# Performance work log

Measured on AMD Instinct MI355X. Metric: run time of the kernel, lower is better.

The kernel has to match this reference:

```python
import jax, jax.numpy as jnp
import numpy as np

B, T, D = 8, 1024, 512
H = 8
F_OUT = D // H          # 64 per head
ALPHA = 0.2             # LeakyReLU slope in GAT
MASK_RATE = 0.3
GAMMA = 0.0625          # DistanceAdj gamma
BIAS = 0.2              # DistanceAdj bias
LN_EPS = 1e-5
NEG_INF = -9e15
L2_EPS = 1e-12          # F.normalize eps


def setup_inputs() -> dict:
    key = jax.random.key(0)
    ks = jax.random.split(key, 8)
    return {
        "x": jax.random.normal(ks[0], (B, T, D), jnp.float32),
        "W": jax.random.normal(ks[1], (H, D, F_OUT), jnp.float32) * 0.05,
        "a_src": jax.random.normal(ks[2], (H, F_OUT), jnp.float32) * 0.05,
        "a_dst": jax.random.normal(ks[3], (H, F_OUT), jnp.float32) * 0.05,
        "W2": jax.random.normal(ks[4], (D, D), jnp.float32) * 0.02,
        "b2": jnp.zeros((D,), jnp.float32),
        "ln_g": jnp.ones((D,), jnp.float32),
        "ln_b": jnp.zeros((D,), jnp.float32),
    }


def _distance_adj(batch, t):
    # DistanceAdj: Gaussian kernel over temporal index distance, shared across batch
    idx = jnp.arange(t, dtype=jnp.float32)
    d2 = (idx[:, None] - idx[None, :]) ** 2
    adj = jnp.exp(-GAMMA * d2 - BIAS)                      # [T, T]
    return jnp.broadcast_to(adj[None], (batch, t, t))      # [B, T, T]


def reference(x, W, a_src, a_dst, W2, b2, ln_g, ln_b):
    b, t, d = x.shape
    adj = _distance_adj(b, t)

    # top-k magnitude node selection -> row/col union mask (index_fill loop)
    k = int(MASK_RATE * t)
    mags = jnp.linalg.norm(x, axis=2)                      # [B, T]
    _, topk = jax.lax.top_k(mags, k)                       # [B, k]
    sel = jnp.zeros((b, t), bool).at[jnp.arange(b)[:, None], topk].set(True)
    mask = sel[:, :, None] | sel[:, None, :]               # rows OR cols filled
    adj = jnp.where(mask, adj, 0.0)

    # GAT multi-head attention (dense masked form, dropout=0 at eval)
    Wh = jnp.einsum("btd,hdf->bhtf", x, W)                 # [B,H,T,F']
    e_src = jnp.einsum("bhtf,hf->bht", Wh, a_src)
    e_dst = jnp.einsum("bhtf,hf->bht", Wh, a_dst)
    e = jax.nn.leaky_relu(e_src[..., :, None] + e_dst[..., None, :], ALPHA)
    e = jnp.where(adj[:, None] > 0, e, NEG_INF)            # masked logits
    attn = jax.nn.softmax(e, axis=-1)                      # [B,H,T,T]
    hp = jnp.einsum("bhts,bhsf->bhtf", attn, Wh)
    hp = jax.nn.elu(hp)                                    # concat=True -> elu per head
    tmp = hp.transpose(0, 2, 1, 3).reshape(b, t, d)        # concat heads -> [B,T,512]

    # signed-sqrt + F.normalize (default dim=1 -> over T axis)
    tmp = jnp.sqrt(jax.nn.relu(tmp)) - jnp.sqrt(jax.nn.relu(-tmp))
    nrm = jnp.linalg.norm(tmp, axis=1, keepdims=True)      # [B,1,D]
    tmp = tmp / jnp.maximum(nrm, L2_EPS)

    # residual linear + LayerNorm + permute
    y = x + tmp @ W2 + b2
    mu = jnp.mean(y, axis=-1, keepdims=True)
    var = jnp.mean((y - mu) ** 2, axis=-1, keepdims=True)
    y = (y - mu) / jnp.sqrt(var + LN_EPS) * ln_g + ln_b
    return y.transpose(0, 2, 1)                            # [B, D, T]
```

## Files before the change

### kernel.cpp

```cpp
#include <hip/hip_runtime.h>
#include <hip/hip_bf16.h>

typedef unsigned short u16;
typedef short bf16x8 __attribute__((ext_vector_type(8)));
typedef float f32x4 __attribute__((ext_vector_type(4)));
typedef int   i32x4 __attribute__((ext_vector_type(4)));

#define NB 8
#define NT 1024
#define ND 512
#define KSEL 307
#define PSTR 152
#define TSTR 136

__device__ __forceinline__ float bf2f(u16 u){
  union { unsigned int i; float f; } c; c.i = ((unsigned int)u) << 16; return c.f;
}
__device__ __forceinline__ u16 f2bf(float f){
  __hip_bfloat16 h = __float2bfloat16(f);
  u16 u; __builtin_memcpy(&u, &h, 2); return u;
}

__global__ void k_convert_w(const float* __restrict__ W, const float* __restrict__ W2,
                            u16* __restrict__ WcatT, u16* __restrict__ W2T){
  int idx = blockIdx.x * 256 + threadIdx.x;
  if (idx < 262144){
    int c = idx >> 9, d = idx & 511;
    int src = ((c >> 6) << 15) | (d << 6) | (c & 63);
    WcatT[idx] = f2bf(W[src]);
  } else {
    int i = idx - 262144;
    int n = i >> 9, k = i & 511;
    W2T[i] = f2bf(W2[(k << 9) | n]);
  }
}

__global__ void k_select(const float* __restrict__ mags, int* __restrict__ sel){
  __shared__ float sm[NT];
  int b = blockIdx.x;
  int tid = threadIdx.x;
  for (int i = tid; i < NT; i += 256) sm[i] = mags[b * NT + i];
  __syncthreads();
  int tl = tid >> 2, tq = tid & 3;
  int t = blockIdx.y * 64 + tl;
  float m = sm[t];
  int cnt = 0;
  int s0 = tq * 256;
  for (int s = s0; s < s0 + 256; s++){
    float v = sm[s];
    cnt += (v > m) || (v == m && s < t);
  }
  cnt += __shfl_xor(cnt, 1, 64);
  cnt += __shfl_xor(cnt, 2, 64);
  if (tq == 0) sel[b * NT + t] = (cnt < KSEL) ? 1 : 0;
}

__launch_bounds__(256, 3)
__global__ void k_gemm_wh(const float* __restrict__ x, const u16* __restrict__ Bt,
                          const float* __restrict__ a_src, const float* __restrict__ a_dst,
                          u16* __restrict__ WhT, float* __restrict__ es, float* __restrict__ ed,
                          float* __restrict__ mags){
  __shared__ u16 smem[8704];
  u16* As = smem;
  u16* Bs = smem + 5120;
  int m0 = blockIdx.x * 128;
  int h  = blockIdx.y;
  int tid = threadIdx.x;
  int wv = tid >> 6, lane = tid & 63;
  int quad = lane >> 4, lr = lane & 15;
  f32x4 acc[2][4] = {};
  float sq[2] = {0.f, 0.f};
  for (int kt = 0; kt < 512; kt += 32){
    __syncthreads();
#pragma unroll
    for (int i = 0; i < 2; i++){
      int e = tid * 8 + i * 2048;
      int r = e >> 5, c = e & 31;
      const float* xa = &x[(m0 + r) * 512 + kt + c];
      f32x4 u0 = *(const f32x4*)xa;
      f32x4 u1 = *(const f32x4*)(xa + 4);
      u16 pk[8];
#pragma unroll
      for (int q = 0; q < 4; q++){
        sq[i] += u0[q]*u0[q] + u1[q]*u1[q];
        pk[q] = f2bf(u0[q]); pk[4+q] = f2bf(u1[q]);
      }
      *(bf16x8*)&As[r*40 + c] = *(const bf16x8*)pk;
    }
    {
      int e = tid * 8;
      int r = e >> 5, c = e & 31;
      *(bf16x8*)&Bs[r*40 + c] = *(const bf16x8*)&Bt[(h * 64 + r) * 512 + kt + c];
    }
    __syncthreads();
    bf16x8 af[2], bfr[4];
#pragma unroll
    for (int i = 0; i < 2; i++) af[i] = *(const bf16x8*)&As[(wv*32 + i*16 + lr)*40 + quad*8];
#pragma unroll
    for (int i = 0; i < 4; i++) bfr[i] = *(const bf16x8*)&Bs[(i*16 + lr)*40 + quad*8];
#pragma unroll
    for (int mi = 0; mi < 2; mi++)
#pragma unroll
      for (int ni = 0; ni < 4; ni++)
        acc[mi][ni] = __builtin_amdgcn_mfma_f32_16x16x32_bf16(af[mi], bfr[ni], acc[mi][ni], 0, 0, 0);
  }
  if (blockIdx.y == 0){
#pragma unroll
    for (int i = 0; i < 2; i++){
      float s = sq[i];
      s += __shfl_xor(s, 1, 64);
      s += __shfl_xor(s, 2, 64);
      if ((tid & 3) == 0) mags[m0 + i*64 + (tid >> 2)] = sqrtf(s);
    }
  }
  float asv[4], adv[4];
#pragma unroll
  for (int ni = 0; ni < 4; ni++){
    asv[ni] = a_src[h*64 + ni*16 + lr];
    adv[ni] = a_dst[h*64 + ni*16 + lr];
  }
#pragma unroll
  for (int mi = 0; mi < 2; mi++)
#pragma unroll
    for (int r = 0; r < 4; r++){
      float pes = 0.f, ped = 0.f;
#pragma unroll
      for (int ni = 0; ni < 4; ni++){
        pes += acc[mi][ni][r] * asv[ni];
        ped += acc[mi][ni][r] * adv[ni];
      }
#pragma unroll
      for (int mofs = 1; mofs < 16; mofs <<= 1){
        pes += __shfl_xor(pes, mofs, 64);
        ped += __shfl_xor(ped, mofs, 64);
      }
      if (lr == 0){
        int rowg = m0 + wv*32 + mi*16 + quad*4 + r;
        int bb_ = rowg >> 10, tt = rowg & 1023;
        es[(bb_ * 8 + h) * NT + tt] = pes;
        ed[(bb_ * 8 + h) * NT + tt] = ped;
      }
    }
  __syncthreads();
  u16* Tr = smem;
#pragma unroll
  for (int mi = 0; mi < 2; mi++)
#pragma unroll
    for (int ni = 0; ni < 4; ni++){
      int fl = ni*16 + lr;
      int tl = wv*32 + mi*16 + quad*4;
#pragma unroll
      for (int r = 0; r < 4; r++) Tr[fl*TSTR + tl + r] = f2bf(acc[mi][ni][r]);
    }
  __syncthreads();
  int f = tid >> 2, seg = tid & 3;
  int b_ = m0 >> 10;
  u16* dst = &WhT[(b_ * 512 + h * 64 + f) * NT + (m0 & 1023) + seg*32];
  const u16* srcp = &Tr[f*TSTR + seg*32];
#pragma unroll
  for (int k8 = 0; k8 < 4; k8++)
    *(bf16x8*)(dst + k8*8) = *(const bf16x8*)(srcp + k8*8);
}

__launch_bounds__(256)
__global__ void k_attn(const u16* __restrict__ WhT, const float* __restrict__ es,
                       const float* __restrict__ ed, const int* __restrict__ sel,
                       u16* __restrict__ t2b, float* __restrict__ cn){
  __shared__ u16 P[64 * PSTR];
  __shared__ float edw[144];
  __shared__ int   selw[144];
  __shared__ float esw[64];
  __shared__ float swv[64];
  int bh = blockIdx.x;
  int b = bh >> 3;
  int t0 = blockIdx.y * 64;
  int tid = threadIdx.x;
  int wv = tid >> 6, lane = tid & 63;
  int quad = lane >> 4, lr = lane & 15;
  int s_base = t0 - 40;
  for (int i = tid; i < 144; i += 256){
    int s = s_base + i;
    bool ok = (s >= 0 && s < NT);
    edw[i]  = ok ? ed[bh * NT + s] : 0.f;
    selw[i] = ok ? sel[b * NT + s] : 0;
  }
  if (tid < 64) esw[tid] = es[bh * NT + t0 + tid];
  {
    i32x4 z = {};
    for (int i = lane; i < 304; i += 64){
      int r16 = i / 19, c16 = i - r16 * 19;
      *(i32x4*)&P[(16*wv + r16) * PSTR + c16 * 8] = z;
    }
  }
  __syncthreads();
  {
    int tl = 16*wv + (lane >> 2);
    int q = lane & 3;
    float e_t = esw[tl];
    int sel_t = selw[tl + 40];
    float part = 0.f;
    for (int j = q; j <= 80; j += 4){
      int sw = tl + j;
      int s = s_base + sw;
      float w = 0.f;
      if (s >= 0 && s < NT && (sel_t | selw[sw])){
        float v = e_t + edw[sw];
        v = v > 0.f ? v : 0.2f * v;
        v = fminf(v, 60.f);
        w = bf2f(f2bf(__expf(v)));
      }
      part += w;
      if (w != 0.f) P[tl * PSTR + sw] = f2bf(w);
    }
    part += __shfl_xor(part, 1, 64);
    part += __shfl_xor(part, 2, 64);
    if (q == 0) swv[tl] = part;
  }
  f32x4 acc[4] = {};
  const u16* vbase = WhT + (bh * 64) * NT;
#pragma unroll
  for (int ks = 0; ks < 96; ks += 32){
    bf16x8 afr = *(const bf16x8*)&P[(16*wv + lr) * PSTR + 16*wv + ks + quad*8];
    int tb = s_base + 16*wv + ks + quad*8;
    bool ok = (tb >= 0) && (tb < NT);
    bf16x8 zf = {};
#pragma unroll
    for (int jn = 0; jn < 4; jn++){
      bf16x8 bfr = ok ? *(const bf16x8*)&vbase[(16*jn + lr) * NT + tb] : zf;
      acc[jn] = __builtin_amdgcn_mfma_f32_16x16x32_bf16(afr, bfr, acc[jn], 0, 0, 0);
    }
  }
#pragma unroll
  for (int jn = 0; jn < 4; jn++){
    float ssum = 0.f;
#pragma unroll
    for (int r = 0; r < 4; r++){
      int t_loc = 16*wv + quad*4 + r;
      float sw_ = swv[t_loc];
      float hp = acc[jn][r] / (sw_ > 0.f ? sw_ : 1.f);
      hp = hp > 0.f ? hp : (__expf(hp) - 1.f);
      float o = hp >= 0.f ? sqrtf(hp) : -sqrtf(-hp);
      ssum += o * o;
      t2b[(b * NT + t0 + t_loc) * ND + (bh & 7) * 64 + 16*jn + lr] = f2bf(o);
    }
    ssum += __shfl_xor(ssum, 16, 64);
    ssum += __shfl_xor(ssum, 32, 64);
    if (quad == 0) atomicAdd(&cn[b * ND + (bh & 7) * 64 + 16*jn + lr], ssum);
  }
}

__launch_bounds__(256, 3)
__global__ void k_gemm2(const u16* __restrict__ A, const u16* __restrict__ Bt,
                        const float* __restrict__ xres, const float* __restrict__ b2,
                        const float* __restrict__ cn, float* __restrict__ Y,
                        float* __restrict__ rsum, float* __restrict__ rqsum){
  __shared__ u16 As[128 * 40];
  __shared__ u16 Bs[64 * 40];
  __shared__ float scl[512];
  int m0 = blockIdx.x * 128, n0 = blockIdx.y * 64;
  int tid = threadIdx.x;
  int wv = tid >> 6, lane = tid & 63;
  int quad = lane >> 4, lr = lane & 15;
  int bb0 = (m0 >> 10) << 9;
  for (int i = tid; i < 512; i += 256){
    float nv = sqrtf(cn[bb0 + i]);
    scl[i] = 1.f / fmaxf(nv, 1e-12f);
  }
  f32x4 acc[2][4] = {};
  for (int kt = 0; kt < 512; kt += 32){
    __syncthreads();
#pragma unroll
    for (int i = 0; i < 2; i++){
      int e = tid * 8 + i * 2048;
      int r = e >> 5, c = e & 31;
      bf16x8 raw = *(const bf16x8*)&A[(m0 + r) * 512 + kt + c];
      u16 pk[8];
#pragma unroll
      for (int q = 0; q < 8; q++)
        pk[q] = f2bf(bf2f((u16)raw[q]) * scl[kt + c + q]);
      *(bf16x8*)&As[r*40 + c] = *(const bf16x8*)pk;
    }
    {
      int e = tid * 8;
      int r = e >> 5, c = e & 31;
      *(bf16x8*)&Bs[r*40 + c] = *(const bf16x8*)&Bt[(n0 + r) * 512 + kt + c];
    }
    __syncthreads();
    bf16x8 af[2], bfr[4];
#pragma unroll
    for (int i = 0; i < 2; i++) af[i] = *(const bf16x8*)&As[(wv*32 + i*16 + lr)*40 + quad*8];
#pragma unroll
    for (int i = 0; i < 4; i++) bfr[i] = *(const bf16x8*)&Bs[(i*16 + lr)*40 + quad*8];
#pragma unroll
    for (int mi = 0; mi < 2; mi++)
#pragma unroll
      for (int ni = 0; ni < 4; ni++)
        acc[mi][ni] = __builtin_amdgcn_mfma_f32_16x16x32_bf16(af[mi], bfr[ni], acc[mi][ni], 0, 0, 0);
  }
  float b2v[4];
#pragma unroll
  for (int ni = 0; ni < 4; ni++) b2v[ni] = b2[n0 + ni*16 + lr];
#pragma unroll
  for (int mi = 0; mi < 2; mi++){
    int rgb = m0 + wv*32 + mi*16 + quad*4;
#pragma unroll
    for (int r = 0; r < 4; r++){
      int row = rgb + r;
      float rs = 0.f, rq = 0.f;
#pragma unroll
      for (int ni = 0; ni < 4; ni++){
        int cg = n0 + ni*16 + lr;
        int idx = row * 512 + cg;
        float yv = acc[mi][ni][r] + xres[idx] + b2v[ni];
        Y[idx] = yv;
        rs += yv; rq += yv * yv;
      }
#pragma unroll
      for (int m2 = 1; m2 < 16; m2 <<= 1){
        rs += __shfl_xor(rs, m2, 64);
        rq += __shfl_xor(rq, m2, 64);
      }
      if (lr == 0){
        atomicAdd(&rsum[row], rs);
        atomicAdd(&rqsum[row], rq);
      }
    }
  }
}

__global__ void k_outln(const float* __restrict__ Y, const float* __restrict__ rsum,
                        const float* __restrict__ rqsum, const float* __restrict__ g,
                        const float* __restrict__ bb, float* __restrict__ out){
  __shared__ float mus[64], rss[64];
  __shared__ float tile[64 * 65];
  int t0 = blockIdx.x * 64, b = blockIdx.y;
  int cbase = blockIdx.z * 128;
  int tid = threadIdx.x;
  if (tid < 64){
    int row = b * NT + t0 + tid;
    float m = rsum[row] * (1.f/512.f);
    float var = rqsum[row] * (1.f/512.f) - m * m;
    mus[tid] = m;
    rss[tid] = 1.f / sqrtf(var + 1e-5f);
  }
  __syncthreads();
  int j = tid & 63, i0 = tid >> 6;
  for (int c0 = cbase; c0 < cbase + 128; c0 += 64){
#pragma unroll
    for (int k = 0; k < 16; k++){
      int i = i0 + k * 4;
      float v = (Y[(b * NT + t0 + i) * ND + c0 + j] - mus[i]) * rss[i] * g[c0 + j] + bb[c0 + j];
      tile[i * 65 + j] = v;
    }
    __syncthreads();
#pragma unroll
    for (int k = 0; k < 16; k++){
      int jj = i0 + k * 4;
      out[(b * ND + c0 + jj) * NT + t0 + j] = tile[j * 65 + jj];
    }
    __syncthreads();
  }
}

extern "C" void kernel_launch(void* const* d_in, const int* in_sizes, int n_in,
                              void* d_out, int out_size, void* d_ws, size_t ws_size,
                              hipStream_t stream) {
  (void)in_sizes; (void)n_in; (void)out_size; (void)ws_size;
  const float* x     = (const float*)d_in[0];
  const float* W     = (const float*)d_in[1];
  const float* a_src = (const float*)d_in[2];
  const float* a_dst = (const float*)d_in[3];
  const float* W2    = (const float*)d_in[4];
  const float* b2    = (const float*)d_in[5];
  const float* ln_g  = (const float*)d_in[6];
  const float* ln_b  = (const float*)d_in[7];
  char* ws = (char*)d_ws;
  int*   sel   = (int*)  (ws + 256);
  float* mags  = (float*)(ws + 33024);
  u16*   WcatT = (u16*)  (ws + 65792);
  u16*   W2T   = (u16*)  (ws + 590080);
  float* es    = (float*)(ws + 1124608);
  float* ed    = (float*)(ws + 1386752);
  float* cn    = (float*)(ws + 1648896);
  float* rsum  = (float*)(ws + 1665280);
  float* rqsum = (float*)(ws + 1698048);
  u16*   WhT   = (u16*)  (ws + 2097152);
  u16*   t2b   = (u16*)  (ws + 18874368);
  float* Y     = (float*)(ws + 2097152);
  float* out   = (float*)d_out;

  k_convert_w<<<2048, 256, 0, stream>>>(W, W2, WcatT, W2T);
  hipMemsetAsync(cn, 0, 81920, stream);
  k_gemm_wh  <<<dim3(64, 8), 256, 0, stream>>>(x, WcatT, a_src, a_dst, WhT, es, ed, mags);
  k_select   <<<dim3(NB, 16), 256, 0, stream>>>(mags, sel);
  k_attn     <<<dim3(64, 16), 256, 0, stream>>>(WhT, es, ed, sel, t2b, cn);
  k_gemm2    <<<dim3(64, 8), 256, 0, stream>>>(t2b, W2T, x, b2, cn, Y, rsum, rqsum);
  k_outln    <<<dim3(16, NB, 4), 256, 0, stream>>>(Y, rsum, rqsum, ln_g, ln_b, out);
}
```

Measured before the change: 161.1 us.

## Fuse second GEMM with LayerNorm and transposed output write

Replaces the tiled output-projection GEMM plus separate LayerNorm/transpose kernel with one kernel in which each block computes full 512-wide rows for 32 tokens. The row statistics are reduced in shared memory instead of with global atomics, and the normalized tile is transposed through LDS and written out directly. This removes the Y intermediate round trip, the atomics and one launch. In exchange the grid shrinks to 256 blocks, each block re-streams all of W2, and LDS usage rises, lowering occupancy.

```diff
diff --git a/kernel.cpp b/kernel.cpp
--- a/kernel.cpp
+++ b/kernel.cpp
@@ -12,6 +12,8 @@
 #define KSEL 307
 #define PSTR 152
 #define TSTR 136
+#define AS2 520
+#define BS2 36
 
 __device__ __forceinline__ float bf2f(u16 u){
   union { unsigned int i; float f; } c; c.i = ((unsigned int)u) << 16; return c.f;
@@ -249,116 +251,133 @@
   }
 }
 
-__launch_bounds__(256, 3)
-__global__ void k_gemm2(const u16* __restrict__ A, const u16* __restrict__ Bt,
-                        const float* __restrict__ xres, const float* __restrict__ b2,
-                        const float* __restrict__ cn, float* __restrict__ Y,
-                        float* __restrict__ rsum, float* __restrict__ rqsum){
-  __shared__ u16 As[128 * 40];
-  __shared__ u16 Bs[64 * 40];
+__launch_bounds__(256, 2)
+__global__ void k_gemm2out(const u16* __restrict__ A, const u16* __restrict__ Bt,
+                           const float* __restrict__ xres, const float* __restrict__ b2,
+                           const float* __restrict__ cn, const float* __restrict__ g,
+                           const float* __restrict__ bb, float* __restrict__ out){
+  __shared__ i32x4 smemQ[4384];
   __shared__ float scl[512];
-  int m0 = blockIdx.x * 128, n0 = blockIdx.y * 64;
+  __shared__ float sS[128], sQ[128];
+  __shared__ float mus[32], rss[32];
+  u16* As = (u16*)smemQ;
+  u16* Bs = (u16*)smemQ + 16640;
+  float* tile = (float*)smemQ;
+  int m0 = blockIdx.x * 32;
+  int b  = m0 >> 10;
+  int t0 = m0 & 1023;
   int tid = threadIdx.x;
-  int wv = tid >> 6, lane = tid & 63;
+  int w = tid >> 6, lane = tid & 63;
   int quad = lane >> 4, lr = lane & 15;
-  int bb0 = (m0 >> 10) << 9;
+  int bb0 = b << 9;
   for (int i = tid; i < 512; i += 256){
     float nv = sqrtf(cn[bb0 + i]);
     scl[i] = 1.f / fmaxf(nv, 1e-12f);
   }
-  f32x4 acc[2][4] = {};
+  __syncthreads();
+  {
+    int row = tid >> 3, seg = tid & 7;
+    const u16* src = &A[(size_t)(m0 + row) * 512 + seg * 64];
+    u16* dstl = &As[row * AS2 + seg * 64];
+#pragma unroll
+    for (int j = 0; j < 8; j++){
+      bf16x8 raw = *(const bf16x8*)(src + j*8);
+      u16 pk[8];
+#pragma unroll
+      for (int e = 0; e < 8; e++)
+        pk[e] = f2bf(bf2f((u16)raw[e]) * scl[seg*64 + j*8 + e]);
+      *(bf16x8*)(dstl + j*8) = *(const bf16x8*)pk;
+    }
+  }
+  f32x4 acc[2][8] = {};
   for (int kt = 0; kt < 512; kt += 32){
     __syncthreads();
 #pragma unroll
-    for (int i = 0; i < 2; i++){
-      int e = tid * 8 + i * 2048;
-      int r = e >> 5, c = e & 31;
-      bf16x8 raw = *(const bf16x8*)&A[(m0 + r) * 512 + kt + c];
-      u16 pk[8];
-#pragma unroll
-      for (int q = 0; q < 8; q++)
-        pk[q] = f2bf(bf2f((u16)raw[q]) * scl[kt + c + q]);
-      *(bf16x8*)&As[r*40 + c] = *(const bf16x8*)pk;
-    }
-    {
-      int e = tid * 8;
-      int r = e >> 5, c = e & 31;
-      *(bf16x8*)&Bs[r*40 + c] = *(const bf16x8*)&Bt[(n0 + r) * 512 + kt + c];
+    for (int half = 0; half < 2; half++){
+      int n = tid + half*256;
+      const u16* src = &Bt[(size_t)n * 512 + kt];
+      u16* dstl = &Bs[n * BS2];
+#pragma unroll
+      for (int j = 0; j < 4; j++)
+        *(bf16x8*)(dstl + j*8) = *(const bf16x8*)(src + j*8);
     }
     __syncthreads();
-    bf16x8 af[2], bfr[4];
-#pragma unroll
-    for (int i = 0; i < 2; i++) af[i] = *(const bf16x8*)&As[(wv*32 + i*16 + lr)*40 + quad*8];
-#pragma unroll
-    for (int i = 0; i < 4; i++) bfr[i] = *(const bf16x8*)&Bs[(i*16 + lr)*40 + quad*8];
-#pragma unroll
-    for (int mi = 0; mi < 2; mi++)
-#pragma unroll
-      for (int ni = 0; ni < 4; ni++)
-        acc[mi][ni] = __builtin_amdgcn_mfma_f32_16x16x32_bf16(af[mi], bfr[ni], acc[mi][ni], 0, 0, 0);
-  }
-  float b2v[4];
-#pragma unroll
-  for (int ni = 0; ni < 4; ni++) b2v[ni] = b2[n0 + ni*16 + lr];
-#pragma unroll
-  for (int mi = 0; mi < 2; mi++){
-    int rgb = m0 + wv*32 + mi*16 + quad*4;
+    bf16x8 af0 = *(const bf16x8*)&As[lr * AS2 + kt + quad*8];
+    bf16x8 af1 = *(const bf16x8*)&As[(16 + lr) * AS2 + kt + quad*8];
+#pragma unroll
+    for (int ni = 0; ni < 8; ni++){
+      bf16x8 bfr = *(const bf16x8*)&Bs[(w*128 + ni*16 + lr)*BS2 + quad*8];
+      acc[0][ni] = __builtin_amdgcn_mfma_f32_16x16x32_bf16(af0, bfr, acc[0][ni], 0, 0, 0);
+      acc[1][ni] = __builtin_amdgcn_mfma_f32_16x16x32_bf16(af1, bfr, acc[1][ni], 0, 0, 0);
+    }
+  }
+  float b2v[8];
+#pragma unroll
+  for (int ni = 0; ni < 8; ni++) b2v[ni] = b2[w*128 + ni*16 + lr];
+#pragma unroll
+  for (int mi = 0; mi < 2; mi++)
 #pragma unroll
     for (int r = 0; r < 4; r++){
-      int row = rgb + r;
+      int row = mi*16 + quad*4 + r;
       float rs = 0.f, rq = 0.f;
 #pragma unroll
-      for (int ni = 0; ni < 4; ni++){
-        int cg = n0 + ni*16 + lr;
-        int idx = row * 512 + cg;
-        float yv = acc[mi][ni][r] + xres[idx] + b2v[ni];
-        Y[idx] = yv;
+      for (int ni = 0; ni < 8; ni++){
+        int col = w*128 + ni*16 + lr;
+        float yv = acc[mi][ni][r] + xres[(size_t)(m0 + row) * 512 + col] + b2v[ni];
+        acc[mi][ni][r] = yv;
         rs += yv; rq += yv * yv;
       }
 #pragma unroll
-      for (int m2 = 1; m2 < 16; m2 <<= 1){
-        rs += __shfl_xor(rs, m2, 64);
-        rq += __shfl_xor(rq, m2, 64);
-      }
-      if (lr == 0){
-        atomicAdd(&rsum[row], rs);
-        atomicAdd(&rqsum[row], rq);
-      }
-    }
-  }
-}
-
-__global__ void k_outln(const float* __restrict__ Y, const float* __restrict__ rsum,
-                        const float* __restrict__ rqsum, const float* __restrict__ g,
-                        const float* __restrict__ bb, float* __restrict__ out){
-  __shared__ float mus[64], rss[64];
-  __shared__ float tile[64 * 65];
-  int t0 = blockIdx.x * 64, b = blockIdx.y;
-  int cbase = blockIdx.z * 128;
-  int tid = threadIdx.x;
-  if (tid < 64){
-    int row = b * NT + t0 + tid;
-    float m = rsum[row] * (1.f/512.f);
-    float var = rqsum[row] * (1.f/512.f) - m * m;
+      for (int mo = 1; mo < 16; mo <<= 1){
+        rs += __shfl_xor(rs, mo, 64);
+        rq += __shfl_xor(rq, mo, 64);
+      }
+      if (lr == 0){ sS[row*4 + w] = rs; sQ[row*4 + w] = rq; }
+    }
+  __syncthreads();
+  if (tid < 32){
+    float s = sS[tid*4] + sS[tid*4+1] + sS[tid*4+2] + sS[tid*4+3];
+    float q = sQ[tid*4] + sQ[tid*4+1] + sQ[tid*4+2] + sQ[tid*4+3];
+    float m = s * (1.f/512.f);
+    float var = q * (1.f/512.f) - m * m;
     mus[tid] = m;
     rss[tid] = 1.f / sqrtf(var + 1e-5f);
   }
   __syncthreads();
-  int j = tid & 63, i0 = tid >> 6;
-  for (int c0 = cbase; c0 < cbase + 128; c0 += 64){
-#pragma unroll
-    for (int k = 0; k < 16; k++){
-      int i = i0 + k * 4;
-      float v = (Y[(b * NT + t0 + i) * ND + c0 + j] - mus[i]) * rss[i] * g[c0 + j] + bb[c0 + j];
-      tile[i * 65 + j] = v;
-    }
-    __syncthreads();
-#pragma unroll
-    for (int k = 0; k < 16; k++){
-      int jj = i0 + k * 4;
-      out[(b * ND + c0 + jj) * NT + t0 + j] = tile[j * 65 + jj];
-    }
-    __syncthreads();
+  float gv[8], bv[8];
+#pragma unroll
+  for (int ni = 0; ni < 8; ni++){
+    gv[ni] = g[w*128 + ni*16 + lr];
+    bv[ni] = bb[w*128 + ni*16 + lr];
+  }
+#pragma unroll
+  for (int mi = 0; mi < 2; mi++)
+#pragma unroll
+    for (int r = 0; r < 4; r++){
+      int row = mi*16 + quad*4 + r;
+      float mu_ = mus[row], rs_ = rss[row];
+#pragma unroll
+      for (int ni = 0; ni < 8; ni++){
+        int col = w*128 + ni*16 + lr;
+        tile[col*33 + row] = (acc[mi][ni][r] - mu_) * rs_ * gv[ni] + bv[ni];
+      }
+    }
+  __syncthreads();
+  {
+    size_t obase = (size_t)b * 512 * 1024 + t0;
+#pragma unroll
+    for (int cc = 0; cc < 2; cc++){
+      int col = tid*2 + cc;
+      const float* srcp = &tile[col*33];
+      float* dst = &out[obase + (size_t)col * 1024];
+#pragma unroll
+      for (int j = 0; j < 8; j++){
+        f32x4 v;
+#pragma unroll
+        for (int e = 0; e < 4; e++) v[e] = srcp[j*4 + e];
+        *(f32x4*)(dst + j*4) = v;
+      }
+    }
   }
 }
 
@@ -382,18 +401,14 @@
   float* es    = (float*)(ws + 1124608);
   float* ed    = (float*)(ws + 1386752);
   float* cn    = (float*)(ws + 1648896);
-  float* rsum  = (float*)(ws + 1665280);
-  float* rqsum = (float*)(ws + 1698048);
   u16*   WhT   = (u16*)  (ws + 2097152);
   u16*   t2b   = (u16*)  (ws + 18874368);
-  float* Y     = (float*)(ws + 2097152);
   float* out   = (float*)d_out;
 
   k_convert_w<<<2048, 256, 0, stream>>>(W, W2, WcatT, W2T);
-  hipMemsetAsync(cn, 0, 81920, stream);
+  hipMemsetAsync(cn, 0, 16384, stream);
   k_gemm_wh  <<<dim3(64, 8), 256, 0, stream>>>(x, WcatT, a_src, a_dst, WhT, es, ed, mags);
   k_select   <<<dim3(NB, 16), 256, 0, stream>>>(mags, sel);
   k_attn     <<<dim3(64, 16), 256, 0, stream>>>(WhT, es, ed, sel, t2b, cn);
-  k_gemm2    <<<dim3(64, 8), 256, 0, stream>>>(t2b, W2T, x, b2, cn, Y, rsum, rqsum);
-  k_outln    <<<dim3(16, NB, 4), 256, 0, stream>>>(Y, rsum, rqsum, ln_g, ln_b, out);
-}
+  k_gemm2out <<<256, 256, 0, stream>>>(t2b, W2T, x, b2, cn, ln_g, ln_b, out);
+}
```

Result: slower. 181.9 us (+12.9%).
